# Kernel tuning notes

Hardware: AMD Instinct MI355X
Metric: run time of the kernel (lower is better)

Reference implementation:

```python
import jax, jax.numpy as jnp
import numpy as np

EPS = 1e-12  # undefined global `eps` in the original source; standard tiny epsilon


def setup_inputs() -> dict:
    key = jax.random.key(0)
    k1, k2 = jax.random.split(key)
    B, C = 32768, 1000
    output = jax.random.normal(k1, (B, C), dtype=jnp.float32)
    multilabels = (jax.random.uniform(k2, (B, C)) < 0.05).astype(jnp.float32)
    multilabels = multilabels.at[:, 0].set(1.0)
    return {"output": output, "multilabels": multilabels}


def reference(output, multilabels):
    # Equivalent closed form of: for every nonempty subset g of true labels,
    #   loss(g) = -[ pseudo_y*log(o+eps) + (1-pseudo_y)*log(1-o+eps) ].sum()
    #           = base - sum_{j in g} gain_j,
    # with base = -sum_j log(1-o_j+eps) and gain_j = log(o_j+eps)-log(1-o_j+eps).
    # min over nonempty subsets = base - max nonempty-subset gain
    #   = base - (sum of positive gains over true labels, or the max single
    #      gain among true labels if all gains are negative).
    o = jax.nn.sigmoid(output)                      # [B, C]
    log_p = jnp.log(o + EPS)
    log_np = jnp.log(1.0 - o + EPS)
    base = -jnp.sum(log_np, axis=1)                 # [B]
    gain = log_p - log_np                           # [B, C]
    is_true = multilabels == 1.0                    # [B, C] bool (constant)
    pos = is_true & (gain > 0)
    pos_gain = jnp.sum(jnp.where(pos, gain, 0.0), axis=1)          # [B]
    any_pos = jnp.any(pos, axis=1)                                  # [B]
    best_single = jnp.max(jnp.where(is_true, gain, -jnp.inf), axis=1)  # [B]
    max_gain = jnp.where(any_pos, pos_gain, best_single)
    per_sample = base - max_gain                    # [B]
    return jnp.mean(per_sample)
```

## Files before the change

kernel.cpp:

```cpp
#include <hip/hip_runtime.h>
#include <math.h>


constexpr int B = 32768;
constexpr int C = 1000;
constexpr int C4 = C / 4;
constexpr int THREADS = 256;

__device__ __forceinline__ void elem_update(float x, float m,
                                            float& base, float& pos, float& best) {
    float e  = __expf(-fabsf(x));
    float xp = fmaxf(x, 0.0f);
    base += xp + __logf(1.0f + e);
    pos  += m * xp;
    if (m != 0.0f) best = fmaxf(best, x);
}

__global__ __launch_bounds__(THREADS)
void row_loss_kernel(const float* __restrict__ X,
                     const float* __restrict__ M,
                     float* __restrict__ partial) {
    const int row = blockIdx.x;
    const int t   = threadIdx.x;

    float base = 0.f, pos = 0.f, best = -INFINITY;

    if (t < C4) {
        const float4* x4 = reinterpret_cast<const float4*>(X + (size_t)row * C);
        const float4* m4 = reinterpret_cast<const float4*>(M + (size_t)row * C);
        float4 x = x4[t];
        float4 m = m4[t];
        elem_update(x.x, m.x, base, pos, best);
        elem_update(x.y, m.y, base, pos, best);
        elem_update(x.z, m.z, base, pos, best);
        elem_update(x.w, m.w, base, pos, best);
    }

    #pragma unroll
    for (int off = 32; off > 0; off >>= 1) {
        base += __shfl_down(base, off, 64);
        pos  += __shfl_down(pos,  off, 64);
        best  = fmaxf(best, __shfl_down(best, off, 64));
    }

    __shared__ float sb[4], sp[4], ss[4];
    const int w    = t >> 6;
    const int lane = t & 63;
    if (lane == 0) { sb[w] = base; sp[w] = pos; ss[w] = best; }
    __syncthreads();
    if (t == 0) {
        float b = (sb[0] + sb[1]) + (sb[2] + sb[3]);
        float p = (sp[0] + sp[1]) + (sp[2] + sp[3]);
        float s = fmaxf(fmaxf(ss[0], ss[1]), fmaxf(ss[2], ss[3]));
        partial[row] = b - ((p > 0.f) ? p : s);
    }
}

__global__ __launch_bounds__(256)
void finalize_kernel(const float* __restrict__ partial, float* __restrict__ out) {
    double t = 0.0;
    for (int i = threadIdx.x; i < B; i += 256) t += (double)partial[i];

    #pragma unroll
    for (int off = 32; off > 0; off >>= 1)
        t += __shfl_down(t, off, 64);

    __shared__ double s[4];
    const int lane = threadIdx.x & 63;
    const int w    = threadIdx.x >> 6;
    if (lane == 0) s[w] = t;
    __syncthreads();
    if (threadIdx.x == 0) {
        double r = (s[0] + s[1]) + (s[2] + s[3]);
        out[0] = (float)(r / (double)B);
    }
}

extern "C" void kernel_launch(void* const* d_in, const int* in_sizes, int n_in,
                              void* d_out, int out_size, void* d_ws, size_t ws_size,
                              hipStream_t stream) {
    const float* X  = (const float*)d_in[0];
    const float* M  = (const float*)d_in[1];
    float* out      = (float*)d_out;
    float* partial  = (float*)d_ws;

    row_loss_kernel<<<B, THREADS, 0, stream>>>(X, M, partial);
    finalize_kernel<<<1, 256, 0, stream>>>(partial, out);
}
```

Before: 293.0 us.

## Load rows via global_load_lds into LDS and fold final reduction into atomics

Each block now stages its row of logits and labels directly into LDS using the global_load_lds builtin, then reads float4 values from LDS instead of issuing direct global loads. The separate finalize kernel is replaced by a per-row float atomicAdd of the scaled per-sample loss into the output, with a tiny kernel that zeroes the output first. This is meant to remove the second reduction pass and change how loads are issued, at the cost of 32768 same-address atomics and a nondeterministic float accumulation order with lower precision than the old double reduction.

Result: slower. 599.2 us (+104.5%).

```diff
diff --git a/kernel.cpp b/kernel.cpp
--- a/kernel.cpp
+++ b/kernel.cpp
@@ -6,6 +6,9 @@
 constexpr int C = 1000;
 constexpr int C4 = C / 4;
 constexpr int THREADS = 256;
+
+typedef float GF __attribute__((address_space(1)));
+typedef float LF __attribute__((address_space(3)));
 
 __device__ __forceinline__ void elem_update(float x, float m,
                                             float& base, float& pos, float& best) {
@@ -16,20 +19,41 @@
     if (m != 0.0f) best = fmaxf(best, x);
 }
 
+__global__ void zero_out(float* __restrict__ out) {
+    if (threadIdx.x == 0) out[0] = 0.0f;
+}
+
 __global__ __launch_bounds__(THREADS)
 void row_loss_kernel(const float* __restrict__ X,
                      const float* __restrict__ M,
-                     float* __restrict__ partial) {
-    const int row = blockIdx.x;
-    const int t   = threadIdx.x;
+                     float* __restrict__ out) {
+    __shared__ float4 ldsX[256];
+    __shared__ float4 ldsM[256];
+
+    const int row  = blockIdx.x;
+    const int t    = threadIdx.x;
+    const int w    = t >> 6;
+    const int lane = t & 63;
+
+    const float* xrow = X + (size_t)row * C;
+    const float* mrow = M + (size_t)row * C;
+
+    {
+        const float* gx = xrow + w * 256 + lane * 4;
+        const float* gm = mrow + w * 256 + lane * 4;
+        LF* lx = (LF*)((float*)ldsX + w * 256);
+        LF* lm = (LF*)((float*)ldsM + w * 256);
+        if (w < 3 || lane < 58) {
+            __builtin_amdgcn_global_load_lds((const GF*)gx, lx, 16, 0, 0);
+            __builtin_amdgcn_global_load_lds((const GF*)gm, lm, 16, 0, 0);
+        }
+    }
+    __syncthreads();
 
     float base = 0.f, pos = 0.f, best = -INFINITY;
-
     if (t < C4) {
-        const float4* x4 = reinterpret_cast<const float4*>(X + (size_t)row * C);
-        const float4* m4 = reinterpret_cast<const float4*>(M + (size_t)row * C);
-        float4 x = x4[t];
-        float4 m = m4[t];
+        float4 x = ldsX[t];
+        float4 m = ldsM[t];
         elem_update(x.x, m.x, base, pos, best);
         elem_update(x.y, m.y, base, pos, best);
         elem_update(x.z, m.z, base, pos, best);
@@ -44,46 +68,24 @@
     }
 
     __shared__ float sb[4], sp[4], ss[4];
-    const int w    = t >> 6;
-    const int lane = t & 63;
     if (lane == 0) { sb[w] = base; sp[w] = pos; ss[w] = best; }
     __syncthreads();
     if (t == 0) {
         float b = (sb[0] + sb[1]) + (sb[2] + sb[3]);
         float p = (sp[0] + sp[1]) + (sp[2] + sp[3]);
         float s = fmaxf(fmaxf(ss[0], ss[1]), fmaxf(ss[2], ss[3]));
-        partial[row] = b - ((p > 0.f) ? p : s);
-    }
-}
-
-__global__ __launch_bounds__(256)
-void finalize_kernel(const float* __restrict__ partial, float* __restrict__ out) {
-    double t = 0.0;
-    for (int i = threadIdx.x; i < B; i += 256) t += (double)partial[i];
-
-    #pragma unroll
-    for (int off = 32; off > 0; off >>= 1)
-        t += __shfl_down(t, off, 64);
-
-    __shared__ double s[4];
-    const int lane = threadIdx.x & 63;
-    const int w    = threadIdx.x >> 6;
-    if (lane == 0) s[w] = t;
-    __syncthreads();
-    if (threadIdx.x == 0) {
-        double r = (s[0] + s[1]) + (s[2] + s[3]);
-        out[0] = (float)(r / (double)B);
+        float per = b - ((p > 0.f) ? p : s);
+        atomicAdd(out, per * (1.0f / (float)B));
     }
 }
 
 extern "C" void kernel_launch(void* const* d_in, const int* in_sizes, int n_in,
                               void* d_out, int out_size, void* d_ws, size_t ws_size,
                               hipStream_t stream) {
-    const float* X  = (const float*)d_in[0];
-    const float* M  = (const float*)d_in[1];
-    float* out      = (float*)d_out;
-    float* partial  = (float*)d_ws;
+    const float* X = (const float*)d_in[0];
+    const float* M = (const float*)d_in[1];
+    float* out     = (float*)d_out;
 
-    row_loss_kernel<<<B, THREADS, 0, stream>>>(X, M, partial);
-    finalize_kernel<<<1, 256, 0, stream>>>(partial, out);
+    zero_out<<<1, 64, 0, stream>>>(out);
+    row_loss_kernel<<<B, THREADS, 0, stream>>>(X, M, out);
 }
```
